# Performance work log

Measured on AMD Instinct MI355X. Metric: run time of the kernel, lower is better.

Reference implementation:

```python
import jax, jax.numpy as jnp
import numpy as np

B, NINP, NCLS = 16384, 2048, 100


def setup_inputs() -> dict:
    key = jax.random.key(0)
    k1, k2, k3, k4, k5 = jax.random.split(key, 5)
    s = 1.0 / np.sqrt(NINP)
    return {
        "time_series": jax.random.normal(k1, (B, NINP), jnp.float32),
        "w_weight": jax.random.uniform(k2, (NINP, NINP), jnp.float32, -s, s),
        "w_bias": jax.random.uniform(k3, (NINP,), jnp.float32, -s, s),
        "fc_weight": jax.random.uniform(k4, (NCLS, NINP), jnp.float32, -s, s),
        "fc_bias": jax.random.uniform(k5, (NCLS,), jnp.float32, -s, s),
    }


def reference(time_series, w_weight, w_bias, fc_weight, fc_bias):
    # time_series: [B, N]
    n = time_series.shape[1]
    # gamma = cumsum(softmax(w(x), axis=1), axis=1): monotone warp in (0, 1]
    gamma = jnp.cumsum(jax.nn.softmax(time_series @ w_weight.T + w_bias, axis=1), axis=1)
    # Interp1d(linspace(0,1,N), x, gamma): per-row linear interpolation,
    # sampling each series at the warped time points gamma.
    xs = jnp.linspace(0.0, 1.0, n, dtype=time_series.dtype)  # shared knot grid
    warped = jax.vmap(lambda g, y: jnp.interp(g, xs, y))(gamma, time_series)  # [B, N]
    return warped @ fc_weight.T + fc_bias  # [B, nclasses]
```

## Files before the change

kernel.cpp:

```cpp
#include <hip/hip_runtime.h>
#include <hip/hip_bf16.h>

#define BROWS 16384
#define NDIM  2048
#define NCLS  100

typedef __attribute__((ext_vector_type(8))) __bf16 bf16x8;
typedef __attribute__((ext_vector_type(4))) float f32x4;
typedef __attribute__((ext_vector_type(16))) float f32x16;
typedef __attribute__((ext_vector_type(4))) unsigned short u16x4;
typedef __attribute__((ext_vector_type(8))) unsigned short u16x8;

__device__ __forceinline__ unsigned short f2bf(float f) {
    union { float f; unsigned int u; } v; v.f = f;
    unsigned int u = v.u;
    unsigned int r = (u + 0x7fffu + ((u >> 16) & 1u)) >> 16;
    return (unsigned short)r;
}
__device__ __forceinline__ float bf2f(unsigned short h) {
    union { unsigned int u; float f; } v; v.u = ((unsigned int)h) << 16;
    return v.f;
}

#define GLOAD_LDS(g, l) \
    __builtin_amdgcn_global_load_lds((const __attribute__((address_space(1))) void*)(g), \
                                     (__attribute__((address_space(3))) void*)(l), 16, 0, 0)

__global__ __launch_bounds__(256) void prep_kernel(const float4* __restrict__ x,
                                                   const float4* __restrict__ w,
                                                   u16x4* __restrict__ xhi, u16x4* __restrict__ xlo,
                                                   u16x4* __restrict__ whi, u16x4* __restrict__ wlo,
                                                   int n4x, int n4w)
{
    int i = blockIdx.x * 256 + threadIdx.x;
    const float4* src; u16x4 *hi, *lo; int idx;
    if (i < n4x) { src = x; hi = xhi; lo = xlo; idx = i; }
    else { idx = i - n4x; if (idx >= n4w) return; src = w; hi = whi; lo = wlo; }
    float4 v = src[idx];
    u16x4 h, l;
    h.x = f2bf(v.x); l.x = f2bf(v.x - bf2f(h.x));
    h.y = f2bf(v.y); l.y = f2bf(v.y - bf2f(h.y));
    h.z = f2bf(v.z); l.z = f2bf(v.z - bf2f(h.z));
    h.w = f2bf(v.w); l.w = f2bf(v.w - bf2f(h.w));
    hi[idx] = h; lo[idx] = l;
}

__global__ __launch_bounds__(256) void cvt_bf16_kernel(const float4* __restrict__ src,
                                                       u16x4* __restrict__ dst, int n4)
{
    int i = blockIdx.x * 256 + threadIdx.x;
    if (i >= n4) return;
    float4 v = src[i];
    u16x4 h;
    h.x = f2bf(v.x); h.y = f2bf(v.y); h.z = f2bf(v.z); h.w = f2bf(v.w);
    dst[i] = h;
}

__global__ __launch_bounds__(256) void gemm1_mfma_fused_kernel(
        const unsigned short* __restrict__ xhi,
        const unsigned short* __restrict__ xlo,
        const unsigned short* __restrict__ whi,
        const unsigned short* __restrict__ wlo,
        const float* __restrict__ bias,
        float* __restrict__ C)
{
    __shared__ unsigned short sAh[128 * 32];
    __shared__ unsigned short sAl[128 * 32];
    __shared__ unsigned short sBh[128 * 32];
    __shared__ unsigned short sBl[128 * 32];

    const int tid  = threadIdx.x;
    const int lane = tid & 63;
    const int w    = tid >> 6;
    const int wm   = w & 1;
    const int wn   = w >> 1;
    const int m0   = blockIdx.y * 128;
    const int n0   = blockIdx.x * 128;

    const int c0 = w * 128 + lane;
    const int r0 = c0 >> 2;
    const int q0 = (c0 & 3) ^ ((r0 >> 1) & 3);
    const int c1 = c0 + 64;
    const int r1 = c1 >> 2;
    const int q1 = (c1 & 3) ^ ((r1 >> 1) & 3);

    const size_t a_goff0 = (size_t)(m0 + r0) * NDIM + q0 * 8;
    const size_t a_goff1 = (size_t)(m0 + r1) * NDIM + q1 * 8;
    const size_t b_goff0 = (size_t)(n0 + r0) * NDIM + q0 * 8;
    const size_t b_goff1 = (size_t)(n0 + r1) * NDIM + q1 * 8;

    unsigned short* ldsAh0 = &sAh[w * 1024];   unsigned short* ldsAh1 = &sAh[w * 1024 + 512];
    unsigned short* ldsAl0 = &sAl[w * 1024];   unsigned short* ldsAl1 = &sAl[w * 1024 + 512];
    unsigned short* ldsBh0 = &sBh[w * 1024];   unsigned short* ldsBh1 = &sBh[w * 1024 + 512];
    unsigned short* ldsBl0 = &sBl[w * 1024];   unsigned short* ldsBl1 = &sBl[w * 1024 + 512];

    const int ln32 = lane & 31;
    const int lk2  = lane >> 5;
    int offA[2][2], offB[2][2];
#pragma unroll
    for (int i = 0; i < 2; i++) {
#pragma unroll
        for (int ks = 0; ks < 2; ks++) {
            int ra = wm * 64 + i * 32 + ln32;
            offA[i][ks] = ra * 32 + (((2 * ks + lk2) ^ ((ra >> 1) & 3)) * 8);
            int rb = wn * 64 + i * 32 + ln32;
            offB[i][ks] = rb * 32 + (((2 * ks + lk2) ^ ((rb >> 1) & 3)) * 8);
        }
    }

    f32x16 acc[2][2];
#pragma unroll
    for (int i = 0; i < 2; i++)
#pragma unroll
        for (int j = 0; j < 2; j++)
#pragma unroll
            for (int r = 0; r < 16; r++) acc[i][j][r] = 0.f;

    for (int kt = 0; kt < NDIM; kt += 32) {
        GLOAD_LDS(xhi + a_goff0 + kt, ldsAh0);
        GLOAD_LDS(xhi + a_goff1 + kt, ldsAh1);
        GLOAD_LDS(xlo + a_goff0 + kt, ldsAl0);
        GLOAD_LDS(xlo + a_goff1 + kt, ldsAl1);
        GLOAD_LDS(whi + b_goff0 + kt, ldsBh0);
        GLOAD_LDS(whi + b_goff1 + kt, ldsBh1);
        GLOAD_LDS(wlo + b_goff0 + kt, ldsBl0);
        GLOAD_LDS(wlo + b_goff1 + kt, ldsBl1);
        __syncthreads();

#pragma unroll
        for (int ks = 0; ks < 2; ks++) {
            bf16x8 ah[2], al[2], bh[2], bl[2];
#pragma unroll
            for (int i = 0; i < 2; i++) {
                ah[i] = *(const bf16x8*)&sAh[offA[i][ks]];
                al[i] = *(const bf16x8*)&sAl[offA[i][ks]];
                bh[i] = *(const bf16x8*)&sBh[offB[i][ks]];
                bl[i] = *(const bf16x8*)&sBl[offB[i][ks]];
            }
#pragma unroll
            for (int i = 0; i < 2; i++)
#pragma unroll
                for (int j = 0; j < 2; j++) {
                    acc[i][j] = __builtin_amdgcn_mfma_f32_32x32x16_bf16(ah[i], bh[j], acc[i][j], 0, 0, 0);
                    acc[i][j] = __builtin_amdgcn_mfma_f32_32x32x16_bf16(ah[i], bl[j], acc[i][j], 0, 0, 0);
                    acc[i][j] = __builtin_amdgcn_mfma_f32_32x32x16_bf16(al[i], bh[j], acc[i][j], 0, 0, 0);
                }
        }
        __syncthreads();
    }

    float bb[2];
#pragma unroll
    for (int j = 0; j < 2; j++) bb[j] = bias[n0 + wn * 64 + j * 32 + ln32];
#pragma unroll
    for (int i = 0; i < 2; i++) {
#pragma unroll
        for (int j = 0; j < 2; j++) {
            const int n = n0 + wn * 64 + j * 32 + ln32;
#pragma unroll
            for (int reg = 0; reg < 16; reg++) {
                const int m = m0 + wm * 64 + i * 32 + (reg & 3) + 8 * (reg >> 2) + 4 * lk2;
                C[(size_t)m * NDIM + n] = acc[i][j][reg] + bb[j];
            }
        }
    }
}

__global__ __launch_bounds__(256) void warp_bf16_kernel(const float* __restrict__ X,
                                                        const float* __restrict__ L,
                                                        unsigned short* __restrict__ Wout)
{
    const int N = NDIM;
    const int row = blockIdx.x;
    const int tid = threadIdx.x;
    const int lane = tid & 63;
    const int wave = tid >> 6;

    __shared__ float s_x[NDIM];
    __shared__ float s_red[4];
    __shared__ float s_wsum[4];

    const float* lrow = L + (size_t)row * N;
    const float* xrow = X + (size_t)row * N;

    float v[8];
    {
        float4 l0 = *(const float4*)(lrow + tid * 8);
        float4 l1 = *(const float4*)(lrow + tid * 8 + 4);
        v[0] = l0.x; v[1] = l0.y; v[2] = l0.z; v[3] = l0.w;
        v[4] = l1.x; v[5] = l1.y; v[6] = l1.z; v[7] = l1.w;
        float4 x0 = *(const float4*)(xrow + tid * 8);
        float4 x1 = *(const float4*)(xrow + tid * 8 + 4);
        *(float4*)&s_x[tid * 8]     = x0;
        *(float4*)&s_x[tid * 8 + 4] = x1;
    }

    float mx = v[0];
#pragma unroll
    for (int j = 1; j < 8; j++) mx = fmaxf(mx, v[j]);
#pragma unroll
    for (int off = 32; off > 0; off >>= 1) mx = fmaxf(mx, __shfl_down(mx, off));
    if (lane == 0) s_red[wave] = mx;
    __syncthreads();
    mx = fmaxf(fmaxf(s_red[0], s_red[1]), fmaxf(s_red[2], s_red[3]));

    float c = 0.0f;
#pragma unroll
    for (int j = 0; j < 8; j++) {
        float e = __expf(v[j] - mx);
        c += e;
        v[j] = c;
    }

    float sc = c;
#pragma unroll
    for (int off = 1; off < 64; off <<= 1) {
        float t = __shfl_up(sc, off);
        if (lane >= off) sc += t;
    }
    if (lane == 63) s_wsum[wave] = sc;
    __syncthreads();
    float base = 0.0f, total = 0.0f;
#pragma unroll
    for (int w = 0; w < 4; w++) {
        float t = s_wsum[w];
        if (w < wave) base += t;
        total += t;
    }
    const float inv = 1.0f / total;
    const float prefix = base + (sc - c);

    u16x8 o;
#pragma unroll
    for (int j = 0; j < 8; j++) {
        float g = (prefix + v[j]) * inv;
        float pos = g * (float)(N - 1);
        pos = fminf(fmaxf(pos, 0.0f), (float)(N - 1));
        int i = (int)pos;
        if (i > N - 2) i = N - 2;
        float f = pos - (float)i;
        o[j] = f2bf(fmaf(f, s_x[i + 1] - s_x[i], s_x[i]));
    }
    *(u16x8*)(Wout + (size_t)row * N + tid * 8) = o;
}

__global__ __launch_bounds__(256) void gemm2_mfma_kernel(
        const unsigned short* __restrict__ Wp,
        const unsigned short* __restrict__ F,
        const float* __restrict__ fb,
        float* __restrict__ out)
{
    __shared__ unsigned short sA[32 * 64];
    __shared__ unsigned short sB[128 * 64];

    const int tid  = threadIdx.x;
    const int lane = tid & 63;
    const int w    = tid >> 6;
    const int wm   = w & 1;
    const int wn   = w >> 1;
    const int m0   = blockIdx.x * 32;

    const int ca = w * 64 + lane;
    const int ra = ca >> 3;
    const int qa = (ca & 7) ^ (ra & 7);
    const size_t a_goff = (size_t)(m0 + ra) * NDIM + qa * 8;
    unsigned short* ldsA = &sA[w * 512];

    size_t b_goff[4];
    unsigned short* ldsB[4];
#pragma unroll
    for (int t = 0; t < 4; t++) {
        const int cb = t * 256 + w * 64 + lane;
        const int rb = cb >> 3;
        const int qb = (cb & 7) ^ (rb & 7);
        b_goff[t] = (size_t)(rb < NCLS ? rb : NCLS - 1) * NDIM + qb * 8;
        ldsB[t] = &sB[(size_t)t * 2048 + w * 512];
    }

    const int lm = lane & 15;
    const int lk = lane >> 4;
    int offA[2], offB[4][2];
#pragma unroll
    for (int ks = 0; ks < 2; ks++) {
        int r = wm * 16 + lm;
        offA[ks] = r * 64 + (((4 * ks + lk) ^ (r & 7)) * 8);
    }
#pragma unroll
    for (int j = 0; j < 4; j++)
#pragma unroll
        for (int ks = 0; ks < 2; ks++) {
            int r = wn * 64 + j * 16 + lm;
            offB[j][ks] = r * 64 + (((4 * ks + lk) ^ (r & 7)) * 8);
        }

    f32x4 acc[4];
#pragma unroll
    for (int j = 0; j < 4; j++) acc[j] = (f32x4){0.f, 0.f, 0.f, 0.f};

    for (int kt = 0; kt < NDIM; kt += 64) {
        GLOAD_LDS(Wp + a_goff + kt, ldsA);
#pragma unroll
        for (int t = 0; t < 4; t++) GLOAD_LDS(F + b_goff[t] + kt, ldsB[t]);
        __syncthreads();

#pragma unroll
        for (int ks = 0; ks < 2; ks++) {
            bf16x8 af = *(const bf16x8*)&sA[offA[ks]];
            bf16x8 bf[4];
#pragma unroll
            for (int j = 0; j < 4; j++) bf[j] = *(const bf16x8*)&sB[offB[j][ks]];
#pragma unroll
            for (int j = 0; j < 4; j++)
                acc[j] = __builtin_amdgcn_mfma_f32_16x16x32_bf16(af, bf[j], acc[j], 0, 0, 0);
        }
        __syncthreads();
    }

    const int cn = lane & 15;
    const int rg = lane >> 4;
#pragma unroll
    for (int j = 0; j < 4; j++) {
        const int n = wn * 64 + j * 16 + cn;
        if (n < NCLS) {
            const float bbn = fb[n];
#pragma unroll
            for (int reg = 0; reg < 4; reg++) {
                const int m = m0 + wm * 16 + rg * 4 + reg;
                out[(size_t)m * NCLS + n] = acc[j][reg] + bbn;
            }
        }
    }
}

__global__ __launch_bounds__(256) void gemm1_kernel(const float* __restrict__ X,
                                                    const float* __restrict__ W,
                                                    const float* __restrict__ bias,
                                                    float* __restrict__ C)
{
    const int K = NDIM;
    __shared__ float sA[16][128];
    __shared__ float sB[16][128];
    const int tid = threadIdx.x;
    const int tx = tid & 15;
    const int ty = tid >> 4;
    const int m0 = blockIdx.y * 128;
    const int n0 = blockIdx.x * 128;
    float acc[8][8];
#pragma unroll
    for (int i = 0; i < 8; i++)
#pragma unroll
        for (int j = 0; j < 8; j++) acc[i][j] = 0.0f;
    const int s_m = tid >> 1;
    const int s_c = (tid & 1) * 8;
    const float* Ag = X + (size_t)(m0 + s_m) * K + s_c;
    const float* Bg = W + (size_t)(n0 + s_m) * K + s_c;
    for (int kt = 0; kt < K; kt += 16) {
        float4 av0 = *(const float4*)(Ag + kt);
        float4 av1 = *(const float4*)(Ag + kt + 4);
        float4 bv0 = *(const float4*)(Bg + kt);
        float4 bv1 = *(const float4*)(Bg + kt + 4);
        __syncthreads();
        sA[s_c + 0][s_m] = av0.x; sA[s_c + 1][s_m] = av0.y;
        sA[s_c + 2][s_m] = av0.z; sA[s_c + 3][s_m] = av0.w;
        sA[s_c + 4][s_m] = av1.x; sA[s_c + 5][s_m] = av1.y;
        sA[s_c + 6][s_m] = av1.z; sA[s_c + 7][s_m] = av1.w;
        sB[s_c + 0][s_m] = bv0.x; sB[s_c + 1][s_m] = bv0.y;
        sB[s_c + 2][s_m] = bv0.z; sB[s_c + 3][s_m] = bv0.w;
        sB[s_c + 4][s_m] = bv1.x; sB[s_c + 5][s_m] = bv1.y;
        sB[s_c + 6][s_m] = bv1.z; sB[s_c + 7][s_m] = bv1.w;
        __syncthreads();
#pragma unroll
        for (int k = 0; k < 16; k++) {
            float4 a0 = *(const float4*)&sA[k][ty * 8];
            float4 a1 = *(const float4*)&sA[k][ty * 8 + 4];
            float4 b0 = *(const float4*)&sB[k][tx * 8];
            float4 b1 = *(const float4*)&sB[k][tx * 8 + 4];
            float a[8] = {a0.x, a0.y, a0.z, a0.w, a1.x, a1.y, a1.z, a1.w};
            float b[8] = {b0.x, b0.y, b0.z, b0.w, b1.x, b1.y, b1.z, b1.w};
#pragma unroll
            for (int i = 0; i < 8; i++)
#pragma unroll
                for (int j = 0; j < 8; j++)
                    acc[i][j] = fmaf(a[i], b[j], acc[i][j]);
        }
    }
    float bb[8];
#pragma unroll
    for (int j = 0; j < 8; j++) bb[j] = bias[n0 + tx * 8 + j];
#pragma unroll
    for (int i = 0; i < 8; i++) {
        const int m = m0 + ty * 8 + i;
        float* crow = C + (size_t)m * NDIM + n0 + tx * 8;
        *(float4*)(crow)     = make_float4(acc[i][0] + bb[0], acc[i][1] + bb[1],
                                           acc[i][2] + bb[2], acc[i][3] + bb[3]);
        *(float4*)(crow + 4) = make_float4(acc[i][4] + bb[4], acc[i][5] + bb[5],
                                           acc[i][6] + bb[6], acc[i][7] + bb[7]);
    }
}

__global__ __launch_bounds__(256) void warp_kernel_f32(const float* __restrict__ X,
                                                       float* __restrict__ L)
{
    const int N = NDIM;
    const int row = blockIdx.x;
    const int tid = threadIdx.x;
    const int lane = tid & 63;
    const int wave = tid >> 6;
    __shared__ float s_x[NDIM];
    __shared__ float s_red[4];
    __shared__ float s_wsum[4];
    float* lrow = L + (size_t)row * N;
    const float* xrow = X + (size_t)row * N;
    float v[8];
    {
        float4 l0 = *(const float4*)(lrow + tid * 8);
        float4 l1 = *(const float4*)(lrow + tid * 8 + 4);
        v[0] = l0.x; v[1] = l0.y; v[2] = l0.z; v[3] = l0.w;
        v[4] = l1.x; v[5] = l1.y; v[6] = l1.z; v[7] = l1.w;
        float4 x0 = *(const float4*)(xrow + tid * 8);
        float4 x1 = *(const float4*)(xrow + tid * 8 + 4);
        *(float4*)&s_x[tid * 8]     = x0;
        *(float4*)&s_x[tid * 8 + 4] = x1;
    }
    float mx = v[0];
#pragma unroll
    for (int j = 1; j < 8; j++) mx = fmaxf(mx, v[j]);
#pragma unroll
    for (int off = 32; off > 0; off >>= 1) mx = fmaxf(mx, __shfl_down(mx, off));
    if (lane == 0) s_red[wave] = mx;
    __syncthreads();
    mx = fmaxf(fmaxf(s_red[0], s_red[1]), fmaxf(s_red[2], s_red[3]));
    float c = 0.0f;
#pragma unroll
    for (int j = 0; j < 8; j++) {
        float e = __expf(v[j] - mx);
        c += e;
        v[j] = c;
    }
    float sc = c;
#pragma unroll
    for (int off = 1; off < 64; off <<= 1) {
        float t = __shfl_up(sc, off);
        if (lane >= off) sc += t;
    }
    if (lane == 63) s_wsum[wave] = sc;
    __syncthreads();
    float base = 0.0f, total = 0.0f;
#pragma unroll
    for (int w = 0; w < 4; w++) {
        float t = s_wsum[w];
        if (w < wave) base += t;
        total += t;
    }
    const float inv = 1.0f / total;
    const float prefix = base + (sc - c);
    float w8[8];
#pragma unroll
    for (int j = 0; j < 8; j++) {
        float g = (prefix + v[j]) * inv;
        float pos = g * (float)(N - 1);
        pos = fminf(fmaxf(pos, 0.0f), (float)(N - 1));
        int i = (int)pos;
        if (i > N - 2) i = N - 2;
        float f = pos - (float)i;
        w8[j] = fmaf(f, s_x[i + 1] - s_x[i], s_x[i]);
    }
    *(float4*)(lrow + tid * 8)     = make_float4(w8[0], w8[1], w8[2], w8[3]);
    *(float4*)(lrow + tid * 8 + 4) = make_float4(w8[4], w8[5], w8[6], w8[7]);
}

__global__ __launch_bounds__(256) void gemm2_kernel(const float* __restrict__ Wp,
                                                    const float* __restrict__ F,
                                                    const float* __restrict__ fb,
                                                    float* __restrict__ out)
{
    const int K = NDIM;
    __shared__ float sA[16][64];
    __shared__ float sB[16][128];
    const int tid = threadIdx.x;
    const int tx = tid & 15;
    const int ty = tid >> 4;
    const int m0 = blockIdx.x * 64;
    float acc[4][8];
#pragma unroll
    for (int i = 0; i < 4; i++)
#pragma unroll
        for (int j = 0; j < 8; j++) acc[i][j] = 0.0f;
    const int a_m = tid >> 2;
    const int a_c = (tid & 3) * 4;
    const int b_n = tid >> 1;
    const int b_c = (tid & 1) * 8;
    const bool bvalid = (b_n < NCLS);
    const float* Ag = Wp + (size_t)(m0 + a_m) * K + a_c;
    const float* Bg = F + (size_t)b_n * K + b_c;
    for (int kt = 0; kt < K; kt += 16) {
        float4 av = *(const float4*)(Ag + kt);
        float4 bv0 = make_float4(0.f, 0.f, 0.f, 0.f);
        float4 bv1 = make_float4(0.f, 0.f, 0.f, 0.f);
        if (bvalid) {
            bv0 = *(const float4*)(Bg + kt);
            bv1 = *(const float4*)(Bg + kt + 4);
        }
        __syncthreads();
        sA[a_c + 0][a_m] = av.x; sA[a_c + 1][a_m] = av.y;
        sA[a_c + 2][a_m] = av.z; sA[a_c + 3][a_m] = av.w;
        sB[b_c + 0][b_n] = bv0.x; sB[b_c + 1][b_n] = bv0.y;
        sB[b_c + 2][b_n] = bv0.z; sB[b_c + 3][b_n] = bv0.w;
        sB[b_c + 4][b_n] = bv1.x; sB[b_c + 5][b_n] = bv1.y;
        sB[b_c + 6][b_n] = bv1.z; sB[b_c + 7][b_n] = bv1.w;
        __syncthreads();
#pragma unroll
        for (int k = 0; k < 16; k++) {
            float4 a4 = *(const float4*)&sA[k][ty * 4];
            float4 b0 = *(const float4*)&sB[k][tx * 8];
            float4 b1 = *(const float4*)&sB[k][tx * 8 + 4];
            float a[4] = {a4.x, a4.y, a4.z, a4.w};
            float b[8] = {b0.x, b0.y, b0.z, b0.w, b1.x, b1.y, b1.z, b1.w};
#pragma unroll
            for (int i = 0; i < 4; i++)
#pragma unroll
                for (int j = 0; j < 8; j++)
                    acc[i][j] = fmaf(a[i], b[j], acc[i][j]);
        }
    }
#pragma unroll
    for (int i = 0; i < 4; i++) {
        const int m = m0 + ty * 4 + i;
#pragma unroll
        for (int j = 0; j < 8; j++) {
            const int n = tx * 8 + j;
            if (n < NCLS) out[(size_t)m * NCLS + n] = acc[i][j] + fb[n];
        }
    }
}

extern "C" void kernel_launch(void* const* d_in, const int* in_sizes, int n_in,
                              void* d_out, int out_size, void* d_ws, size_t ws_size,
                              hipStream_t stream) {
    const float* x  = (const float*)d_in[0];
    const float* ww = (const float*)d_in[1];
    const float* wb = (const float*)d_in[2];
    const float* fw = (const float*)d_in[3];
    const float* fb = (const float*)d_in[4];
    float* out = (float*)d_out;

    char* ws = (char*)d_ws;
    float* logits = (float*)ws;
    const size_t LOGITS_B = (size_t)BROWS * NDIM * 4;
    const size_t XBF_B    = (size_t)BROWS * NDIM * 2;
    const size_t WBF_B    = (size_t)NDIM * NDIM * 2;
    unsigned short* xhi = (unsigned short*)(ws + LOGITS_B);
    unsigned short* xlo = (unsigned short*)(ws + LOGITS_B + XBF_B);
    unsigned short* whi = (unsigned short*)(ws + LOGITS_B + 2 * XBF_B);
    unsigned short* wlo = (unsigned short*)(ws + LOGITS_B + 2 * XBF_B + WBF_B);
    unsigned short* wbf = xlo;
    unsigned short* fwb = wlo;
    const size_t WS_NEED = LOGITS_B + 2 * XBF_B + 2 * WBF_B;

    if (ws_size >= WS_NEED) {
        const int n4x = BROWS * NDIM / 4;
        const int n4w = NDIM * NDIM / 4;
        prep_kernel<<<(n4x + n4w + 255) / 256, 256, 0, stream>>>(
            (const float4*)x, (const float4*)ww,
            (u16x4*)xhi, (u16x4*)xlo, (u16x4*)whi, (u16x4*)wlo, n4x, n4w);
        gemm1_mfma_fused_kernel<<<dim3(NDIM / 128, BROWS / 128), 256, 0, stream>>>(
            xhi, xlo, whi, wlo, wb, logits);
        warp_bf16_kernel<<<BROWS, 256, 0, stream>>>(x, logits, wbf);
        cvt_bf16_kernel<<<(NCLS * NDIM / 4 + 255) / 256, 256, 0, stream>>>(
            (const float4*)fw, (u16x4*)fwb, NCLS * NDIM / 4);
        gemm2_mfma_kernel<<<BROWS / 32, 256, 0, stream>>>(wbf, fwb, fb, out);
    } else {
        gemm1_kernel<<<dim3(NDIM / 128, BROWS / 128), 256, 0, stream>>>(x, ww, wb, logits);
        warp_kernel_f32<<<BROWS, 256, 0, stream>>>(x, logits);
        gemm2_kernel<<<BROWS / 64, 256, 0, stream>>>(logits, fw, fb, out);
    }
}
```

Baseline: 699.6 us.

## Switch LDS tiles to k-chunk-major layout, pad warp LDS, enlarge gemm2 M tile

```diff
diff --git a/kernel.cpp b/kernel.cpp
--- a/kernel.cpp
+++ b/kernel.cpp
@@ -64,10 +64,10 @@
         const float* __restrict__ bias,
         float* __restrict__ C)
 {
-    __shared__ unsigned short sAh[128 * 32];
-    __shared__ unsigned short sAl[128 * 32];
-    __shared__ unsigned short sBh[128 * 32];
-    __shared__ unsigned short sBl[128 * 32];
+    __shared__ unsigned short sAh[4096];
+    __shared__ unsigned short sAl[4096];
+    __shared__ unsigned short sBh[4096];
+    __shared__ unsigned short sBl[4096];
 
     const int tid  = threadIdx.x;
     const int lane = tid & 63;
@@ -77,36 +77,29 @@
     const int m0   = blockIdx.y * 128;
     const int n0   = blockIdx.x * 128;
 
-    const int c0 = w * 128 + lane;
-    const int r0 = c0 >> 2;
-    const int q0 = (c0 & 3) ^ ((r0 >> 1) & 3);
-    const int c1 = c0 + 64;
-    const int r1 = c1 >> 2;
-    const int q1 = (c1 & 3) ^ ((r1 >> 1) & 3);
+    const int c0 = w * 64 + lane;
+    const int q0 = c0 >> 7, r0 = c0 & 127;
+    const int c1 = c0 + 256;
+    const int q1 = c1 >> 7, r1 = c1 & 127;
 
     const size_t a_goff0 = (size_t)(m0 + r0) * NDIM + q0 * 8;
     const size_t a_goff1 = (size_t)(m0 + r1) * NDIM + q1 * 8;
     const size_t b_goff0 = (size_t)(n0 + r0) * NDIM + q0 * 8;
     const size_t b_goff1 = (size_t)(n0 + r1) * NDIM + q1 * 8;
 
-    unsigned short* ldsAh0 = &sAh[w * 1024];   unsigned short* ldsAh1 = &sAh[w * 1024 + 512];
-    unsigned short* ldsAl0 = &sAl[w * 1024];   unsigned short* ldsAl1 = &sAl[w * 1024 + 512];
-    unsigned short* ldsBh0 = &sBh[w * 1024];   unsigned short* ldsBh1 = &sBh[w * 1024 + 512];
-    unsigned short* ldsBl0 = &sBl[w * 1024];   unsigned short* ldsBl1 = &sBl[w * 1024 + 512];
+    const int lb0 = w * 512;
+    const int lb1 = 2048 + w * 512;
 
     const int ln32 = lane & 31;
     const int lk2  = lane >> 5;
     int offA[2][2], offB[2][2];
 #pragma unroll
-    for (int i = 0; i < 2; i++) {
+    for (int i = 0; i < 2; i++)
 #pragma unroll
         for (int ks = 0; ks < 2; ks++) {
-            int ra = wm * 64 + i * 32 + ln32;
-            offA[i][ks] = ra * 32 + (((2 * ks + lk2) ^ ((ra >> 1) & 3)) * 8);
-            int rb = wn * 64 + i * 32 + ln32;
-            offB[i][ks] = rb * 32 + (((2 * ks + lk2) ^ ((rb >> 1) & 3)) * 8);
-        }
-    }
+            offA[i][ks] = ((2 * ks + lk2) * 128 + wm * 64 + i * 32 + ln32) * 8;
+            offB[i][ks] = ((2 * ks + lk2) * 128 + wn * 64 + i * 32 + ln32) * 8;
+        }
 
     f32x16 acc[2][2];
 #pragma unroll
@@ -117,14 +110,14 @@
             for (int r = 0; r < 16; r++) acc[i][j][r] = 0.f;
 
     for (int kt = 0; kt < NDIM; kt += 32) {
-        GLOAD_LDS(xhi + a_goff0 + kt, ldsAh0);
-        GLOAD_LDS(xhi + a_goff1 + kt, ldsAh1);
-        GLOAD_LDS(xlo + a_goff0 + kt, ldsAl0);
-        GLOAD_LDS(xlo + a_goff1 + kt, ldsAl1);
-        GLOAD_LDS(whi + b_goff0 + kt, ldsBh0);
-        GLOAD_LDS(whi + b_goff1 + kt, ldsBh1);
-        GLOAD_LDS(wlo + b_goff0 + kt, ldsBl0);
-        GLOAD_LDS(wlo + b_goff1 + kt, ldsBl1);
+        GLOAD_LDS(xhi + a_goff0 + kt, &sAh[lb0]);
+        GLOAD_LDS(xhi + a_goff1 + kt, &sAh[lb1]);
+        GLOAD_LDS(xlo + a_goff0 + kt, &sAl[lb0]);
+        GLOAD_LDS(xlo + a_goff1 + kt, &sAl[lb1]);
+        GLOAD_LDS(whi + b_goff0 + kt, &sBh[lb0]);
+        GLOAD_LDS(whi + b_goff1 + kt, &sBh[lb1]);
+        GLOAD_LDS(wlo + b_goff0 + kt, &sBl[lb0]);
+        GLOAD_LDS(wlo + b_goff1 + kt, &sBl[lb1]);
         __syncthreads();
 
 #pragma unroll
@@ -166,6 +159,8 @@
     }
 }
 
+#define SXI(i) ((i) + ((i) >> 5))
+
 __global__ __launch_bounds__(256) void warp_bf16_kernel(const float* __restrict__ X,
                                                         const float* __restrict__ L,
                                                         unsigned short* __restrict__ Wout)
@@ -176,7 +171,7 @@
     const int lane = tid & 63;
     const int wave = tid >> 6;
 
-    __shared__ float s_x[NDIM];
+    __shared__ float s_x[NDIM + NDIM / 32];
     __shared__ float s_red[4];
     __shared__ float s_wsum[4];
 
@@ -191,8 +186,9 @@
         v[4] = l1.x; v[5] = l1.y; v[6] = l1.z; v[7] = l1.w;
         float4 x0 = *(const float4*)(xrow + tid * 8);
         float4 x1 = *(const float4*)(xrow + tid * 8 + 4);
-        *(float4*)&s_x[tid * 8]     = x0;
-        *(float4*)&s_x[tid * 8 + 4] = x1;
+        const int sb = SXI(tid * 8);
+        *(float4*)&s_x[sb]     = x0;
+        *(float4*)&s_x[sb + 4] = x1;
     }
 
     float mx = v[0];
@@ -239,7 +235,9 @@
         int i = (int)pos;
         if (i > N - 2) i = N - 2;
         float f = pos - (float)i;
-        o[j] = f2bf(fmaf(f, s_x[i + 1] - s_x[i], s_x[i]));
+        float x0 = s_x[SXI(i)];
+        float x1 = s_x[SXI(i + 1)];
+        o[j] = f2bf(fmaf(f, x1 - x0, x0));
     }
     *(u16x8*)(Wout + (size_t)row * N + tid * 8) = o;
 }
@@ -250,7 +248,7 @@
         const float* __restrict__ fb,
         float* __restrict__ out)
 {
-    __shared__ unsigned short sA[32 * 64];
+    __shared__ unsigned short sA[64 * 64];
     __shared__ unsigned short sB[128 * 64];
 
     const int tid  = threadIdx.x;
@@ -258,60 +256,64 @@
     const int w    = tid >> 6;
     const int wm   = w & 1;
     const int wn   = w >> 1;
-    const int m0   = blockIdx.x * 32;
-
-    const int ca = w * 64 + lane;
-    const int ra = ca >> 3;
-    const int qa = (ca & 7) ^ (ra & 7);
-    const size_t a_goff = (size_t)(m0 + ra) * NDIM + qa * 8;
-    unsigned short* ldsA = &sA[w * 512];
-
-    size_t b_goff[4];
-    unsigned short* ldsB[4];
+    const int m0   = blockIdx.x * 64;
+
+    size_t a_goff[2]; int a_lb[2];
+#pragma unroll
+    for (int t = 0; t < 2; t++) {
+        const int c = t * 256 + w * 64 + lane;
+        const int q = c >> 6, r = c & 63;
+        a_goff[t] = (size_t)(m0 + r) * NDIM + q * 8;
+        a_lb[t]   = (t * 256 + w * 64) * 8;
+    }
+    size_t b_goff[4]; int b_lb[4];
 #pragma unroll
     for (int t = 0; t < 4; t++) {
-        const int cb = t * 256 + w * 64 + lane;
-        const int rb = cb >> 3;
-        const int qb = (cb & 7) ^ (rb & 7);
-        b_goff[t] = (size_t)(rb < NCLS ? rb : NCLS - 1) * NDIM + qb * 8;
-        ldsB[t] = &sB[(size_t)t * 2048 + w * 512];
+        const int c = t * 256 + w * 64 + lane;
+        const int q = c >> 7, r = c & 127;
+        b_goff[t] = (size_t)(r < NCLS ? r : NCLS - 1) * NDIM + q * 8;
+        b_lb[t]   = (t * 256 + w * 64) * 8;
     }
 
     const int lm = lane & 15;
     const int lk = lane >> 4;
-    int offA[2], offB[4][2];
-#pragma unroll
-    for (int ks = 0; ks < 2; ks++) {
-        int r = wm * 16 + lm;
-        offA[ks] = r * 64 + (((4 * ks + lk) ^ (r & 7)) * 8);
-    }
+    int offA[2][2], offB[4][2];
+#pragma unroll
+    for (int i = 0; i < 2; i++)
+#pragma unroll
+        for (int ks = 0; ks < 2; ks++)
+            offA[i][ks] = ((ks * 4 + lk) * 64 + wm * 32 + i * 16 + lm) * 8;
 #pragma unroll
     for (int j = 0; j < 4; j++)
 #pragma unroll
+        for (int ks = 0; ks < 2; ks++)
+            offB[j][ks] = ((ks * 4 + lk) * 128 + wn * 64 + j * 16 + lm) * 8;
+
+    f32x4 acc[2][4];
+#pragma unroll
+    for (int i = 0; i < 2; i++)
+#pragma unroll
+        for (int j = 0; j < 4; j++) acc[i][j] = (f32x4){0.f, 0.f, 0.f, 0.f};
+
+    for (int kt = 0; kt < NDIM; kt += 64) {
+#pragma unroll
+        for (int t = 0; t < 2; t++) GLOAD_LDS(Wp + a_goff[t] + kt, &sA[a_lb[t]]);
+#pragma unroll
+        for (int t = 0; t < 4; t++) GLOAD_LDS(F + b_goff[t] + kt, &sB[b_lb[t]]);
+        __syncthreads();
+
+#pragma unroll
         for (int ks = 0; ks < 2; ks++) {
-            int r = wn * 64 + j * 16 + lm;
-            offB[j][ks] = r * 64 + (((4 * ks + lk) ^ (r & 7)) * 8);
-        }
-
-    f32x4 acc[4];
-#pragma unroll
-    for (int j = 0; j < 4; j++) acc[j] = (f32x4){0.f, 0.f, 0.f, 0.f};
-
-    for (int kt = 0; kt < NDIM; kt += 64) {
-        GLOAD_LDS(Wp + a_goff + kt, ldsA);
-#pragma unroll
-        for (int t = 0; t < 4; t++) GLOAD_LDS(F + b_goff[t] + kt, ldsB[t]);
-        __syncthreads();
-
-#pragma unroll
-        for (int ks = 0; ks < 2; ks++) {
-            bf16x8 af = *(const bf16x8*)&sA[offA[ks]];
-            bf16x8 bf[4];
+            bf16x8 af[2], bf[4];
+#pragma unroll
+            for (int i = 0; i < 2; i++) af[i] = *(const bf16x8*)&sA[offA[i][ks]];
 #pragma unroll
             for (int j = 0; j < 4; j++) bf[j] = *(const bf16x8*)&sB[offB[j][ks]];
 #pragma unroll
-            for (int j = 0; j < 4; j++)
-                acc[j] = __builtin_amdgcn_mfma_f32_16x16x32_bf16(af, bf[j], acc[j], 0, 0, 0);
+            for (int i = 0; i < 2; i++)
+#pragma unroll
+                for (int j = 0; j < 4; j++)
+                    acc[i][j] = __builtin_amdgcn_mfma_f32_16x16x32_bf16(af[i], bf[j], acc[i][j], 0, 0, 0);
         }
         __syncthreads();
     }
@@ -319,14 +321,17 @@
     const int cn = lane & 15;
     const int rg = lane >> 4;
 #pragma unroll
-    for (int j = 0; j < 4; j++) {
-        const int n = wn * 64 + j * 16 + cn;
-        if (n < NCLS) {
-            const float bbn = fb[n];
-#pragma unroll
-            for (int reg = 0; reg < 4; reg++) {
-                const int m = m0 + wm * 16 + rg * 4 + reg;
-                out[(size_t)m * NCLS + n] = acc[j][reg] + bbn;
+    for (int i = 0; i < 2; i++) {
+#pragma unroll
+        for (int j = 0; j < 4; j++) {
+            const int n = wn * 64 + j * 16 + cn;
+            if (n < NCLS) {
+                const float bbn = fb[n];
+#pragma unroll
+                for (int reg = 0; reg < 4; reg++) {
+                    const int m = m0 + wm * 32 + i * 16 + rg * 4 + reg;
+                    out[(size_t)m * NCLS + n] = acc[i][j][reg] + bbn;
+                }
             }
         }
     }
@@ -568,7 +573,7 @@
         warp_bf16_kernel<<<BROWS, 256, 0, stream>>>(x, logits, wbf);
         cvt_bf16_kernel<<<(NCLS * NDIM / 4 + 255) / 256, 256, 0, stream>>>(
             (const float4*)fw, (u16x4*)fwb, NCLS * NDIM / 4);
-        gemm2_mfma_kernel<<<BROWS / 32, 256, 0, stream>>>(wbf, fwb, fb, out);
+        gemm2_mfma_kernel<<<BROWS / 64, 256, 0, stream>>>(wbf, fwb, fb, out);
     } else {
         gemm1_kernel<<<dim3(NDIM / 128, BROWS / 128), 256, 0, stream>>>(x, ww, wb, logits);
         warp_kernel_f32<<<BROWS, 256, 0, stream>>>(x, logits);
```

After: 887.5 us. 26.9% more time.
